# Performance work log

Hardware: AMD Instinct MI355X
Metric: run time of the kernel (lower is better)

The kernel has to match this reference:

```python
import jax, jax.numpy as jnp
import numpy as np

N = 4096        # nodes
E = 131072      # edges (avg degree 32)
IN_F = 256      # in_features
OUT_F = 64      # out_features per head
H = 8           # num_heads


def setup_inputs() -> dict:
    key = jax.random.key(0)
    k1, k2, k3, k4 = jax.random.split(key, 4)
    x = jax.random.normal(k1, (N, IN_F), dtype=jnp.float32)
    # xavier-ish scales for the learned params
    W = jax.random.normal(k2, (IN_F, OUT_F * H), dtype=jnp.float32) * 0.06
    a = jax.random.normal(k3, (2 * OUT_F, 1), dtype=jnp.float32) * 0.12
    edge_index = jax.random.randint(k4, (2, E), 0, N, dtype=jnp.int32)
    return {"x": x, "W": W, "a": a, "edge_index": edge_index}


def reference(x, W, a, edge_index):
    n = x.shape[0]
    Wh = (x @ W).reshape(n, H, OUT_F)          # [N, H, F]
    src, dst = edge_index[0], edge_index[1]
    # edge score: cat(Wh[src], Wh[dst]) @ a == Wh[src]@a1 + Wh[dst]@a2
    a1 = a[:OUT_F, 0]                           # [F]
    a2 = a[OUT_F:2 * OUT_F, 0]                  # [F]
    alpha_src = Wh @ a1                         # [N, H]
    alpha_dst = Wh @ a2                         # [N, H]
    edge_e = jax.nn.leaky_relu(alpha_src[src] + alpha_dst[dst], 0.2)  # [E, H]
    # dense scatter exactly as the original module (non-edges stay 0 in softmax)
    attention = jnp.zeros((n, n, H), dtype=x.dtype).at[src, dst].set(edge_e)
    attention = jax.nn.softmax(attention, axis=1)
    # dropout is identity in eval mode
    h_prime = jnp.einsum('nmh,mhf->nhf', attention, Wh)  # [N, H, F]
    return h_prime.reshape(n, H * OUT_F)        # concat=True
```

## Files before the change

kernel.cpp:

```cpp
#include <hip/hip_runtime.h>
#include <hip/hip_bf16.h>

constexpr int NN    = 4096;
constexpr int EE    = 131072;
constexpr int IN_F  = 256;
constexpr int OUT_F = 64;
constexpr int HH    = 8;
constexpr int HF    = OUT_F * HH;
constexpr int CAP   = 128;

typedef __attribute__((ext_vector_type(8))) short bf16x8;
typedef __attribute__((ext_vector_type(4))) float f32x4;

__device__ __forceinline__ unsigned short f2b(float f) {
    unsigned int u = __float_as_uint(f);
    u = u + 0x7FFFu + ((u >> 16) & 1u);
    return (unsigned short)(u >> 16);
}
__device__ __forceinline__ float b2f(unsigned int lo16) {
    return __uint_as_float(lo16 << 16);
}

__global__ __launch_bounds__(256) void gemm_mfma(const float* __restrict__ xf,
                                                 const float* __restrict__ Wf,
                                                 const float* __restrict__ a,
                                                 const int* __restrict__ src,
                                                 const int* __restrict__ dst,
                                                 int* __restrict__ cnt,
                                                 int* __restrict__ csr_dst,
                                                 unsigned short* __restrict__ Whb,
                                                 float* __restrict__ asrc,
                                                 float* __restrict__ adst,
                                                 float* __restrict__ S) {
    __shared__ unsigned short Bhi_s[64][264];
    __shared__ unsigned short Blo_s[64][264];
    __shared__ float Scol[64];
    int b = blockIdx.x;
    int t = threadIdx.x;

    {
        int e = b * 256 + t;
        int s = src[e], d = dst[e];
        int pos = atomicAdd(&cnt[s], 1);
        csr_dst[(s << 7) + pos] = d;
    }

    int m0 = (b >> 3) * 64;
    int n0 = (b & 7) * 64;
    if (t < 64) Scol[t] = 0.f;

#pragma unroll 4
    for (int it = 0; it < 16; ++it) {
        int flat = it * 256 + t;
        int k    = flat >> 4;
        int n4   = flat & 15;
        float4 v = *(const float4*)(Wf + (size_t)k * HF + n0 + n4 * 4);
        float fv[4] = {v.x, v.y, v.z, v.w};
#pragma unroll
        for (int j = 0; j < 4; ++j) {
            unsigned short hi = f2b(fv[j]);
            unsigned short lo = f2b(fv[j] - b2f(hi));
            Bhi_s[n4 * 4 + j][k] = hi;
            Blo_s[n4 * 4 + j][k] = lo;
        }
    }
    __syncthreads();

    int w  = t >> 6;
    int l  = t & 63;
    int kg = l >> 4;
    int ln = l & 15;
    int arow = m0 + w * 16 + ln;

    f32x4 acc[4] = {};

#pragma unroll
    for (int ks = 0; ks < 8; ++ks) {
        size_t aoff = (size_t)arow * 256 + ks * 32 + kg * 8;
        float4 v0 = *(const float4*)(xf + aoff);
        float4 v1 = *(const float4*)(xf + aoff + 4);
        float fv[8] = {v0.x, v0.y, v0.z, v0.w, v1.x, v1.y, v1.z, v1.w};
        bf16x8 ahi, alo;
#pragma unroll
        for (int j = 0; j < 8; ++j) {
            unsigned short hi = f2b(fv[j]);
            ahi[j] = (short)hi;
            alo[j] = (short)f2b(fv[j] - b2f(hi));
        }
#pragma unroll
        for (int nt = 0; nt < 4; ++nt) {
            bf16x8 bhi = *(const bf16x8*)(&Bhi_s[nt * 16 + ln][ks * 32 + kg * 8]);
            bf16x8 blo = *(const bf16x8*)(&Blo_s[nt * 16 + ln][ks * 32 + kg * 8]);
            acc[nt] = __builtin_amdgcn_mfma_f32_16x16x32_bf16(ahi, bhi, acc[nt], 0, 0, 0);
            acc[nt] = __builtin_amdgcn_mfma_f32_16x16x32_bf16(ahi, blo, acc[nt], 0, 0, 0);
            acc[nt] = __builtin_amdgcn_mfma_f32_16x16x32_bf16(alo, bhi, acc[nt], 0, 0, 0);
        }
    }

#pragma unroll
    for (int nt = 0; nt < 4; ++nt)
#pragma unroll
        for (int i = 0; i < 4; ++i) {
            int row = m0 + w * 16 + kg * 4 + i;
            Whb[(size_t)row * HF + n0 + nt * 16 + ln] = f2b(acc[nt][i]);
        }

    int h = n0 >> 6;
    float a1v[4], a2v[4];
#pragma unroll
    for (int nt = 0; nt < 4; ++nt) {
        a1v[nt] = a[nt * 16 + ln];
        a2v[nt] = a[OUT_F + nt * 16 + ln];
    }
#pragma unroll
    for (int i = 0; i < 4; ++i) {
        float p1 = acc[0][i] * a1v[0] + acc[1][i] * a1v[1] +
                   acc[2][i] * a1v[2] + acc[3][i] * a1v[3];
        float p2 = acc[0][i] * a2v[0] + acc[1][i] * a2v[1] +
                   acc[2][i] * a2v[2] + acc[3][i] * a2v[3];
#pragma unroll
        for (int mask = 1; mask < 16; mask <<= 1) {
            p1 += __shfl_xor(p1, mask);
            p2 += __shfl_xor(p2, mask);
        }
        if (ln == 0) {
            int node = m0 + w * 16 + kg * 4 + i;
            asrc[node * HH + h] = p1;
            adst[node * HH + h] = p2;
        }
    }

#pragma unroll
    for (int nt = 0; nt < 4; ++nt) {
        float cs = acc[nt][0] + acc[nt][1] + acc[nt][2] + acc[nt][3];
        cs += __shfl_xor(cs, 16);
        cs += __shfl_xor(cs, 32);
        if (kg == 0) atomicAdd(&Scol[nt * 16 + ln], cs);
    }
    __syncthreads();
    if (t < 64) atomicAdd(&S[n0 + t], Scol[t]);
}

__global__ __launch_bounds__(512) void aggregate_kernel(const unsigned short* __restrict__ Whb,
                                                        const float* __restrict__ asrc,
                                                        const float* __restrict__ adst,
                                                        const float* __restrict__ S,
                                                        const int* __restrict__ cnt,
                                                        const int* __restrict__ csr_dst,
                                                        float* __restrict__ out) {
    __shared__ int           midx[CAP];
    __shared__ unsigned char dupf[CAP];
    __shared__ unsigned int  bmap[NN / 32];
    __shared__ float         wbuf[CAP * HH];
    __shared__ float         as_sh[HH];
    __shared__ float         denom[HH];
    __shared__ float         red[8][HF];
    int i = blockIdx.x;
    int t = threadIdx.x;
    int deg = cnt[i];
    if (deg > CAP) deg = CAP;

    if (t < NN / 32) bmap[t] = 0u;
    if (t < HH) as_sh[t] = asrc[i * HH + t];
    for (int j = t; j < deg; j += 512) midx[j] = csr_dst[(i << 7) + j];
    __syncthreads();

    for (int j = t; j < deg; j += 512) {
        int m = midx[j];
        unsigned int old = atomicOr(&bmap[m >> 5], 1u << (m & 31));
        dupf[j] = (unsigned char)((old >> (m & 31)) & 1u);
    }
    __syncthreads();

    for (int idx = t; idx < deg * HH; idx += 512) {
        int sl = idx >> 3, h = idx & 7;
        float w = 0.f;
        if (!dupf[sl]) {
            float xv = as_sh[h] + adst[midx[sl] * HH + h];
            xv = (xv > 0.f) ? xv : 0.2f * xv;
            w = __expf(xv) - 1.f;
        }
        wbuf[idx] = w;
    }
    __syncthreads();

    if (t < 128) {
        int h = t >> 4, ln = t & 15;
        float p = 0.f;
        for (int sl = ln; sl < deg; sl += 16) p += wbuf[sl * HH + h];
#pragma unroll
        for (int mask = 1; mask < 16; mask <<= 1) p += __shfl_xor(p, mask);
        if (ln == 0) denom[h] = (float)NN + p;
    }
    __syncthreads();

    int g = t >> 6;
    int r = t & 63;
    int h = r >> 3;
    float accv[8] = {};

    int j0 = g, j1 = g + 8;
    uint4 u0 = {0, 0, 0, 0}, u1 = {0, 0, 0, 0};
    float w0 = 0.f, w1 = 0.f;
    if (j0 < deg) {
        w0 = wbuf[j0 * HH + h];
        u0 = *(const uint4*)(Whb + ((size_t)midx[j0] << 9) + (r << 3));
    }
    if (j1 < deg) {
        w1 = wbuf[j1 * HH + h];
        u1 = *(const uint4*)(Whb + ((size_t)midx[j1] << 9) + (r << 3));
    }
    int j = j0;
    while (j < deg) {
        int jn = j + 16;
        uint4 un = {0, 0, 0, 0};
        float wn = 0.f;
        if (jn < deg) {
            wn = wbuf[jn * HH + h];
            un = *(const uint4*)(Whb + ((size_t)midx[jn] << 9) + (r << 3));
        }
        accv[0] += w0 * b2f(u0.x & 0xFFFFu);
        accv[1] += w0 * b2f(u0.x >> 16);
        accv[2] += w0 * b2f(u0.y & 0xFFFFu);
        accv[3] += w0 * b2f(u0.y >> 16);
        accv[4] += w0 * b2f(u0.z & 0xFFFFu);
        accv[5] += w0 * b2f(u0.z >> 16);
        accv[6] += w0 * b2f(u0.w & 0xFFFFu);
        accv[7] += w0 * b2f(u0.w >> 16);
        u0 = u1; w0 = w1;
        u1 = un; w1 = wn;
        j += 8;
    }

    float4 v0 = {accv[0], accv[1], accv[2], accv[3]};
    float4 v1 = {accv[4], accv[5], accv[6], accv[7]};
    *(float4*)(&red[g][r * 8])     = v0;
    *(float4*)(&red[g][r * 8 + 4]) = v1;
    __syncthreads();

    float tot = S[t];
#pragma unroll
    for (int gg = 0; gg < 8; ++gg) tot += red[gg][t];
    out[((size_t)i << 9) + t] = tot / denom[t >> 6];
}

extern "C" void kernel_launch(void* const* d_in, const int* in_sizes, int n_in,
                              void* d_out, int out_size, void* d_ws, size_t ws_size,
                              hipStream_t stream) {
    const float* x  = (const float*)d_in[0];
    const float* W  = (const float*)d_in[1];
    const float* a  = (const float*)d_in[2];
    const int*   ei = (const int*)d_in[3];
    const int* src = ei;
    const int* dst = ei + EE;
    float* out = (float*)d_out;

    char* ws = (char*)d_ws;
    unsigned short* Whb = (unsigned short*)(ws + 0);
    float* asrc     = (float*)(ws + 4194304);
    float* adst     = (float*)(ws + 4325376);
    int*   csr_dst  = (int*)  (ws + 4456448);
    float* S        = (float*)(ws + 6553600);
    int*   cnt      = (int*)  (ws + 6555648);

    hipMemsetAsync(ws + 6553600, 0, 2048 + 16384, stream);

    gemm_mfma<<<512, 256, 0, stream>>>(x, W, a, src, dst,
                                       cnt, csr_dst, Whb, asrc, adst, S);

    aggregate_kernel<<<NN, 512, 0, stream>>>(Whb, asrc, adst, S, cnt, csr_dst, out);
}
```

Measured before the change: 110.5 us.

## Shrink aggregate kernel to one wavefront per node, drop cross-wave reduction

```diff
diff --git a/kernel.cpp b/kernel.cpp
--- a/kernel.cpp
+++ b/kernel.cpp
@@ -141,84 +141,77 @@
     if (t < 64) atomicAdd(&S[n0 + t], Scol[t]);
 }
 
-__global__ __launch_bounds__(512) void aggregate_kernel(const unsigned short* __restrict__ Whb,
-                                                        const float* __restrict__ asrc,
-                                                        const float* __restrict__ adst,
-                                                        const float* __restrict__ S,
-                                                        const int* __restrict__ cnt,
-                                                        const int* __restrict__ csr_dst,
-                                                        float* __restrict__ out) {
-    __shared__ int           midx[CAP];
-    __shared__ unsigned char dupf[CAP];
-    __shared__ unsigned int  bmap[NN / 32];
-    __shared__ float         wbuf[CAP * HH];
-    __shared__ float         as_sh[HH];
-    __shared__ float         denom[HH];
-    __shared__ float         red[8][HF];
+__global__ __launch_bounds__(64) void aggregate_kernel(const unsigned short* __restrict__ Whb,
+                                                       const float* __restrict__ asrc,
+                                                       const float* __restrict__ adst,
+                                                       const float* __restrict__ S,
+                                                       const int* __restrict__ cnt,
+                                                       const int* __restrict__ csr_dst,
+                                                       float* __restrict__ out) {
+    __shared__ int          midx[CAP];
+    __shared__ unsigned int bmap[NN / 32];
+    __shared__ float        wbuf[CAP * HH];
     int i = blockIdx.x;
-    int t = threadIdx.x;
+    int l = threadIdx.x;
     int deg = cnt[i];
     if (deg > CAP) deg = CAP;
 
-    if (t < NN / 32) bmap[t] = 0u;
-    if (t < HH) as_sh[t] = asrc[i * HH + t];
-    for (int j = t; j < deg; j += 512) midx[j] = csr_dst[(i << 7) + j];
-    __syncthreads();
-
-    for (int j = t; j < deg; j += 512) {
+    bmap[l] = 0u;
+    bmap[l + 64] = 0u;
+    if (l < deg)      midx[l]      = csr_dst[(i << 7) + l];
+    if (l + 64 < deg) midx[l + 64] = csr_dst[(i << 7) + l + 64];
+    __syncthreads();
+
+    float4 s0 = *(const float4*)(asrc + i * HH);
+    float4 s1 = *(const float4*)(asrc + i * HH + 4);
+    for (int j = l; j < deg; j += 64) {
         int m = midx[j];
         unsigned int old = atomicOr(&bmap[m >> 5], 1u << (m & 31));
-        dupf[j] = (unsigned char)((old >> (m & 31)) & 1u);
-    }
-    __syncthreads();
-
-    for (int idx = t; idx < deg * HH; idx += 512) {
-        int sl = idx >> 3, h = idx & 7;
-        float w = 0.f;
-        if (!dupf[sl]) {
-            float xv = as_sh[h] + adst[midx[sl] * HH + h];
-            xv = (xv > 0.f) ? xv : 0.2f * xv;
-            w = __expf(xv) - 1.f;
-        }
-        wbuf[idx] = w;
-    }
-    __syncthreads();
-
-    if (t < 128) {
-        int h = t >> 4, ln = t & 15;
-        float p = 0.f;
-        for (int sl = ln; sl < deg; sl += 16) p += wbuf[sl * HH + h];
-#pragma unroll
-        for (int mask = 1; mask < 16; mask <<= 1) p += __shfl_xor(p, mask);
-        if (ln == 0) denom[h] = (float)NN + p;
-    }
-    __syncthreads();
-
-    int g = t >> 6;
-    int r = t & 63;
-    int h = r >> 3;
+        if ((old >> (m & 31)) & 1u) {
+            *(float4*)(&wbuf[j * HH])     = make_float4(0.f, 0.f, 0.f, 0.f);
+            *(float4*)(&wbuf[j * HH + 4]) = make_float4(0.f, 0.f, 0.f, 0.f);
+        } else {
+            float4 d0 = *(const float4*)(adst + m * HH);
+            float4 d1 = *(const float4*)(adst + m * HH + 4);
+            float ev[8] = {s0.x + d0.x, s0.y + d0.y, s0.z + d0.z, s0.w + d0.w,
+                           s1.x + d1.x, s1.y + d1.y, s1.z + d1.z, s1.w + d1.w};
+            float w[8];
+#pragma unroll
+            for (int h = 0; h < 8; ++h) {
+                float xv = ev[h];
+                xv = (xv > 0.f) ? xv : 0.2f * xv;
+                w[h] = __expf(xv) - 1.f;
+            }
+            *(float4*)(&wbuf[j * HH])     = make_float4(w[0], w[1], w[2], w[3]);
+            *(float4*)(&wbuf[j * HH + 4]) = make_float4(w[4], w[5], w[6], w[7]);
+        }
+    }
+    __syncthreads();
+
+    int h = l >> 3;
     float accv[8] = {};
-
-    int j0 = g, j1 = g + 8;
+    float z = 0.f;
+
+    int j0 = 0, j1 = 1;
     uint4 u0 = {0, 0, 0, 0}, u1 = {0, 0, 0, 0};
     float w0 = 0.f, w1 = 0.f;
     if (j0 < deg) {
         w0 = wbuf[j0 * HH + h];
-        u0 = *(const uint4*)(Whb + ((size_t)midx[j0] << 9) + (r << 3));
+        u0 = *(const uint4*)(Whb + ((size_t)midx[j0] << 9) + (l << 3));
     }
     if (j1 < deg) {
         w1 = wbuf[j1 * HH + h];
-        u1 = *(const uint4*)(Whb + ((size_t)midx[j1] << 9) + (r << 3));
-    }
-    int j = j0;
-    while (j < deg) {
-        int jn = j + 16;
+        u1 = *(const uint4*)(Whb + ((size_t)midx[j1] << 9) + (l << 3));
+    }
+    for (int j = 0; j < deg; ++j) {
+        int jn = j + 2;
         uint4 un = {0, 0, 0, 0};
         float wn = 0.f;
         if (jn < deg) {
             wn = wbuf[jn * HH + h];
-            un = *(const uint4*)(Whb + ((size_t)midx[jn] << 9) + (r << 3));
-        }
+            un = *(const uint4*)(Whb + ((size_t)midx[jn] << 9) + (l << 3));
+        }
+        z += w0;
         accv[0] += w0 * b2f(u0.x & 0xFFFFu);
         accv[1] += w0 * b2f(u0.x >> 16);
         accv[2] += w0 * b2f(u0.y & 0xFFFFu);
@@ -229,19 +222,17 @@
         accv[7] += w0 * b2f(u0.w >> 16);
         u0 = u1; w0 = w1;
         u1 = un; w1 = wn;
-        j += 8;
-    }
-
-    float4 v0 = {accv[0], accv[1], accv[2], accv[3]};
-    float4 v1 = {accv[4], accv[5], accv[6], accv[7]};
-    *(float4*)(&red[g][r * 8])     = v0;
-    *(float4*)(&red[g][r * 8 + 4]) = v1;
-    __syncthreads();
-
-    float tot = S[t];
-#pragma unroll
-    for (int gg = 0; gg < 8; ++gg) tot += red[gg][t];
-    out[((size_t)i << 9) + t] = tot / denom[t >> 6];
+    }
+
+    float rz = 1.f / ((float)NN + z);
+    float4 S0 = *(const float4*)(S + l * 8);
+    float4 S1 = *(const float4*)(S + l * 8 + 4);
+    float4 o0 = {(S0.x + accv[0]) * rz, (S0.y + accv[1]) * rz,
+                 (S0.z + accv[2]) * rz, (S0.w + accv[3]) * rz};
+    float4 o1 = {(S1.x + accv[4]) * rz, (S1.y + accv[5]) * rz,
+                 (S1.z + accv[6]) * rz, (S1.w + accv[7]) * rz};
+    *(float4*)(out + ((size_t)i << 9) + l * 8)     = o0;
+    *(float4*)(out + ((size_t)i << 9) + l * 8 + 4) = o1;
 }
 
 extern "C" void kernel_launch(void* const* d_in, const int* in_sizes, int n_in,
@@ -268,5 +259,5 @@
     gemm_mfma<<<512, 256, 0, stream>>>(x, W, a, src, dst,
                                        cnt, csr_dst, Whb, asrc, adst, S);
 
-    aggregate_kernel<<<NN, 512, 0, stream>>>(Whb, asrc, adst, S, cnt, csr_dst, out);
-}
+    aggregate_kernel<<<NN, 64, 0, stream>>>(Whb, asrc, adst, S, cnt, csr_dst, out);
+}
```

New measurement: 105.8 us. 1.04x faster.
